# Kernel optimization log

Measured on AMD Instinct MI355X. Metric: run time of the kernel, lower is better.

## Reference

```python
import jax, jax.numpy as jnp
import numpy as np

N_NODES = 50000
N_EDGES = 600000
IN_F, HID, OUT_F = 602, 128, 41


def _gconv(x, W, b, src, dst, n):
    # DGL GraphConv, norm='both': D_dst^{-1/2} A (D_src^{-1/2} x W) + b
    ones = jnp.ones(src.shape, dtype=x.dtype)
    deg_out = jnp.clip(jax.ops.segment_sum(ones, src, num_segments=n), 1.0)
    deg_in = jnp.clip(jax.ops.segment_sum(ones, dst, num_segments=n), 1.0)
    h = x * jax.lax.rsqrt(deg_out)[:, None]
    h = h @ W  # dense transform first (in_feats > out_feats path)
    agg = jax.ops.segment_sum(h[src], dst, num_segments=n)  # [N, out]
    return agg * jax.lax.rsqrt(deg_in)[:, None] + b


def setup_inputs() -> dict:
    key = jax.random.key(0)
    ks = jax.random.split(key, 8)
    features = jax.random.normal(ks[0], (N_NODES, IN_F), dtype=jnp.float32)
    src = jax.random.randint(ks[1], (N_EDGES,), 0, N_NODES, dtype=jnp.int32)
    dst = jax.random.randint(ks[2], (N_EDGES,), 0, N_NODES, dtype=jnp.int32)
    def glorot(k, fan_in, fan_out):
        s = jnp.sqrt(6.0 / (fan_in + fan_out)).astype(jnp.float32)
        return jax.random.uniform(k, (fan_in, fan_out), jnp.float32, -s, s)
    return {
        'features': features, 'src': src, 'dst': dst,
        'W1': glorot(ks[3], IN_F, HID), 'b1': jnp.zeros((HID,), jnp.float32),
        'W2': glorot(ks[4], HID, HID), 'b2': jnp.zeros((HID,), jnp.float32),
        'W3': glorot(ks[5], HID, HID), 'b3': jnp.zeros((HID,), jnp.float32),
        'Wfc': glorot(ks[6], HID, OUT_F), 'bfc': jnp.zeros((OUT_F,), jnp.float32),
    }


def reference(features, src, dst, W1, b1, W2, b2, W3, b3, Wfc, bfc):
    n = features.shape[0]
    relu = jax.nn.relu
    x = relu(_gconv(features, W1, b1, src, dst, n))  # x = _x
    _x = relu(_gconv(x, W2, b2, src, dst, n))        # branch (layer2)
    x = relu(_gconv(x, W2, b2, src, dst, n))         # main (same layer2)
    x = relu(_gconv(x, W3, b3, src, dst, n))         # layer3
    x = relu(x + _x)                                  # residual + relu
    return x @ Wfc + bfc
```

## Files before the change

### kernel.cpp

```cpp
#include <hip/hip_runtime.h>
#include <hip/hip_bf16.h>

#define NN   50000
#define NE   600000
#define INF  602
#define HID  128
#define OUTF 41
#define NBLK 196

#define HISTB 2344
#define GEMMB 782

typedef __attribute__((ext_vector_type(8))) short bf16x8;
typedef __attribute__((ext_vector_type(4))) float f32x4;
typedef __attribute__((ext_vector_type(2))) float f32x2;

__device__ inline unsigned short f2bf(float x) {
    unsigned u = __float_as_uint(x);
    unsigned r = u + 0x7FFF + ((u >> 16) & 1);
    return (unsigned short)(r >> 16);
}

__device__ inline f32x2 up2(unsigned u) {
    return (f32x2){__uint_as_float(u << 16), __uint_as_float(u & 0xFFFF0000u)};
}

#define GLL16(gp, lp) \
    __builtin_amdgcn_global_load_lds((const __attribute__((address_space(1))) unsigned int*)(gp), \
                                     (__attribute__((address_space(3))) unsigned int*)(lp), 16, 0, 0)

__device__ inline void prep_w_body(const float* __restrict__ W, int K,
                                   unsigned short* __restrict__ out, int total4, int i) {
    if (i >= total4) return;
    int col = i & 127;
    int k4 = (i >> 7) << 2;
    short4 h;
    h.x = (short)f2bf((k4 + 0 < K) ? W[(size_t)(k4 + 0) * HID + col] : 0.f);
    h.y = (short)f2bf((k4 + 1 < K) ? W[(size_t)(k4 + 1) * HID + col] : 0.f);
    h.z = (short)f2bf((k4 + 2 < K) ? W[(size_t)(k4 + 2) * HID + col] : 0.f);
    h.w = (short)f2bf((k4 + 3 < K) ? W[(size_t)(k4 + 3) * HID + col] : 0.f);
    *(short4*)&out[(size_t)(k4 >> 3) * 1024 + col * 8 + (k4 & 7)] = h;
}

__global__ __launch_bounds__(256) void hist_prep_k(const int* __restrict__ src,
                                                   const int* __restrict__ dst,
                                                   int* __restrict__ cnt_out,
                                                   int* __restrict__ cnt_in,
                                                   const float* __restrict__ W1,
                                                   const float* __restrict__ W2,
                                                   const float* __restrict__ W3,
                                                   unsigned short* __restrict__ W1t,
                                                   unsigned short* __restrict__ W2t,
                                                   unsigned short* __restrict__ W3t) {
    int b = blockIdx.x;
    if (b < HISTB) {
        int e = b * 256 + threadIdx.x;
        if (e < NE) {
            atomicAdd(&cnt_out[src[e]], 1);
            atomicAdd(&cnt_in[dst[e]], 1);
        }
    } else {
        int b2 = b - HISTB;
        if (b2 < 80)       prep_w_body(W1, INF, W1t, 20480, b2 * 256 + threadIdx.x);
        else if (b2 < 96)  prep_w_body(W2, HID, W2t, 4096, (b2 - 80) * 256 + threadIdx.x);
        else               prep_w_body(W3, HID, W3t, 4096, (b2 - 96) * 256 + threadIdx.x);
    }
}

__global__ __launch_bounds__(256) void scan1_k(const int* __restrict__ cnt,
                                               int* __restrict__ rowptr,
                                               int* __restrict__ blockSum) {
    __shared__ int tmp[256];
    int tid = threadIdx.x;
    int i = blockIdx.x * 256 + tid;
    int v = (i < NN) ? cnt[i] : 0;
    tmp[tid] = v;
    __syncthreads();
#pragma unroll
    for (int off = 1; off < 256; off <<= 1) {
        int t = (tid >= off) ? tmp[tid - off] : 0;
        __syncthreads();
        tmp[tid] += t;
        __syncthreads();
    }
    if (i < NN) rowptr[i] = tmp[tid] - v;
    if (tid == 255) blockSum[blockIdx.x] = tmp[255];
}

__global__ __launch_bounds__(256) void scan23_k(int* __restrict__ rowptr,
                                                const int* __restrict__ blockSum,
                                                int* __restrict__ wcur,
                                                const int* __restrict__ cnt_out,
                                                const int* __restrict__ cnt_in,
                                                float* __restrict__ rs_out,
                                                float* __restrict__ rs_in) {
    const int tid = threadIdx.x;
    const int bid = blockIdx.x;
    int vAll = (tid < NBLK) ? blockSum[tid] : 0;
    int vPre = (tid < bid) ? vAll : 0;
#pragma unroll
    for (int o = 32; o; o >>= 1) {
        vAll += __shfl_down(vAll, o);
        vPre += __shfl_down(vPre, o);
    }
    __shared__ int sA[4], sP[4];
    if ((tid & 63) == 0) { sA[tid >> 6] = vAll; sP[tid >> 6] = vPre; }
    __syncthreads();
    int offAll = sA[0] + sA[1] + sA[2] + sA[3];
    int offPre = sP[0] + sP[1] + sP[2] + sP[3];
    int i = bid * 256 + tid;
    if (i < NN) {
        int r = rowptr[i] + offPre;
        rowptr[i] = r;
        wcur[i] = r;
        int co = cnt_out[i]; if (co < 1) co = 1;
        int ci = cnt_in[i];  if (ci < 1) ci = 1;
        rs_out[i] = rsqrtf((float)co);
        rs_in[i]  = rsqrtf((float)ci);
    }
    if (bid == NBLK - 1 && tid == 0) rowptr[NN] = offAll;
}

__global__ __launch_bounds__(256) void fill_gemm1_k(const int* __restrict__ src,
                                                    const int* __restrict__ dst,
                                                    int* __restrict__ wcur,
                                                    int* __restrict__ csrsrc,
                                                    const float* __restrict__ A,
                                                    const unsigned short* __restrict__ Wt,
                                                    const float* __restrict__ rs_out,
                                                    unsigned short* __restrict__ H, int n) {
    __shared__ __attribute__((aligned(16))) short As[64 * 136];
    __shared__ __attribute__((aligned(16))) short Bs[16 * 1024];

    if (blockIdx.x < HISTB) {
        int e = blockIdx.x * 256 + threadIdx.x;
        if (e < NE) {
            int p = atomicAdd(&wcur[dst[e]], 1);
            csrsrc[p] = src[e];
        }
        return;
    }

    const int gb = blockIdx.x - HISTB;
    const int tid = threadIdx.x;
    const int wave = tid >> 6;
    const int lane = tid & 63;
    const int quad = lane >> 4;
    const int l16 = lane & 15;
    const int rowBase = gb * 64;
    const int tileBase = rowBase + wave * 16;

    float4 apf[8];
    auto loadA = [&](int ch) {
        int kb = ch * 128;
#pragma unroll
        for (int c = 0; c < 8; ++c) {
            int f = c * 256 + tid;
            int row = f >> 5;
            int kc = (f & 31) << 2;
            int grow = rowBase + row;
            int gk = kb + kc;
            float4 v = {0.f, 0.f, 0.f, 0.f};
            if (grow < n) {
                if (gk + 3 < INF) {
                    v = *(const float4*)(A + (size_t)grow * INF + gk);
                } else {
                    if (gk + 0 < INF) v.x = A[(size_t)grow * INF + gk + 0];
                    if (gk + 1 < INF) v.y = A[(size_t)grow * INF + gk + 1];
                    if (gk + 2 < INF) v.z = A[(size_t)grow * INF + gk + 2];
                }
            }
            apf[c] = v;
        }
    };
    auto storeA = [&]() {
#pragma unroll
        for (int c = 0; c < 8; ++c) {
            int f = c * 256 + tid;
            int row = f >> 5;
            int kc = (f & 31) << 2;
            short4 h;
            h.x = (short)f2bf(apf[c].x); h.y = (short)f2bf(apf[c].y);
            h.z = (short)f2bf(apf[c].z); h.w = (short)f2bf(apf[c].w);
            *(short4*)&As[row * 136 + kc] = h;
        }
    };
    auto issueB = [&](int ch) {
#pragma unroll
        for (int c = 0; c < 8; ++c)
            GLL16(Wt + (size_t)ch * 16384 + c * 2048 + tid * 8, &Bs[c * 2048 + tid * 8]);
    };

    f32x4 acc[8];
#pragma unroll
    for (int j = 0; j < 8; ++j) acc[j] = (f32x4){0.f, 0.f, 0.f, 0.f};

    loadA(0);
    for (int ch = 0; ch < 5; ++ch) {
        __syncthreads();
        issueB(ch);
        storeA();
        __syncthreads();
        if (ch + 1 < 5) loadA(ch + 1);
#pragma unroll
        for (int s = 0; s < 4; ++s) {
            bf16x8 af = *(const bf16x8*)&As[(wave * 16 + l16) * 136 + s * 32 + quad * 8];
            const short* bg = &Bs[(s * 4 + quad) * 1024 + l16 * 8];
#pragma unroll
            for (int nt = 0; nt < 8; ++nt) {
                bf16x8 bf = *(const bf16x8*)(bg + nt * 128);
                acc[nt] = __builtin_amdgcn_mfma_f32_16x16x32_bf16(af, bf, acc[nt], 0, 0, 0);
            }
        }
    }

#pragma unroll
    for (int r = 0; r < 4; ++r) {
        int row = tileBase + quad * 4 + r;
        if (row < n) {
            float ro = rs_out[row];
#pragma unroll
            for (int nt = 0; nt < 8; ++nt)
                H[(size_t)row * HID + nt * 16 + l16] = f2bf(acc[nt][r] * ro);
        }
    }
}

__global__ __launch_bounds__(256) void gemm_hid_k(const unsigned short* __restrict__ A,
                                                  const unsigned short* __restrict__ Wt,
                                                  unsigned short* __restrict__ H, int n) {
    __shared__ __attribute__((aligned(16))) short As[64 * 136];
    __shared__ __attribute__((aligned(16))) short Bs[16384];

    const int tid = threadIdx.x;
    const int wave = tid >> 6;
    const int lane = tid & 63;
    const int quad = lane >> 4;
    const int l16 = lane & 15;
    const int wm = wave >> 1;
    const int wn = wave & 1;
    const int rowBase = blockIdx.x * 64;

#pragma unroll
    for (int c = 0; c < 8; ++c)
        GLL16(Wt + c * 2048 + tid * 8, &Bs[c * 2048 + tid * 8]);

#pragma unroll
    for (int c = 0; c < 4; ++c) {
        int f = c * 256 + tid;
        int row = f >> 4;
        int k16 = (f & 15) << 3;
        int grow = rowBase + row;
        int4 v = {0, 0, 0, 0};
        if (grow < n) v = *(const int4*)(A + (size_t)grow * HID + k16);
        *(int4*)&As[row * 136 + k16] = v;
    }
    __syncthreads();

    f32x4 acc[2][4];
#pragma unroll
    for (int i = 0; i < 2; ++i)
#pragma unroll
        for (int j = 0; j < 4; ++j) acc[i][j] = (f32x4){0.f, 0.f, 0.f, 0.f};

#pragma unroll
    for (int kq = 0; kq < 4; ++kq) {
        bf16x8 af[2], bfr[4];
#pragma unroll
        for (int mt = 0; mt < 2; ++mt)
            af[mt] = *(const bf16x8*)&As[(wm * 32 + mt * 16 + l16) * 136 + kq * 32 + quad * 8];
#pragma unroll
        for (int nt = 0; nt < 4; ++nt)
            bfr[nt] = *(const bf16x8*)&Bs[(kq * 4 + quad) * 1024 + (wn * 64 + nt * 16 + l16) * 8];
#pragma unroll
        for (int mt = 0; mt < 2; ++mt)
#pragma unroll
            for (int nt = 0; nt < 4; ++nt)
                acc[mt][nt] = __builtin_amdgcn_mfma_f32_16x16x32_bf16(af[mt], bfr[nt], acc[mt][nt], 0, 0, 0);
    }

#pragma unroll
    for (int mt = 0; mt < 2; ++mt)
#pragma unroll
        for (int r = 0; r < 4; ++r) {
            int row = rowBase + wm * 32 + mt * 16 + quad * 4 + r;
            if (row < n) {
#pragma unroll
                for (int nt = 0; nt < 4; ++nt) {
                    int col = wn * 64 + nt * 16 + l16;
                    H[(size_t)row * HID + col] = f2bf(acc[mt][nt][r]);
                }
            }
        }
}

__global__ __launch_bounds__(256) void gather_k(const unsigned short* __restrict__ H,
                                                const int* __restrict__ rowptr,
                                                const int* __restrict__ csrsrc,
                                                const float* __restrict__ rs_in,
                                                const float* __restrict__ rs_out,
                                                const float* __restrict__ bias,
                                                const float* __restrict__ resid,
                                                float* __restrict__ outX,
                                                unsigned short* __restrict__ outXs,
                                                int n) {
    const int lane = threadIdx.x & 63;
    const int g = lane >> 4;
    const int l = lane & 15;
    const int gbase = g << 4;
    const int wid = blockIdx.x * 4 + (threadIdx.x >> 6);
    const int node = wid * 4 + g;
    const bool alive = node < n;

    int beg = 0, end = 0;
    if (alive) { beg = rowptr[node]; end = rowptr[node + 1]; }

    f32x2 a01 = {0.f, 0.f}, a23 = {0.f, 0.f}, a45 = {0.f, 0.f}, a67 = {0.f, 0.f};

    for (int base = beg; base < end; base += 16) {
        int m = end - base; if (m > 16) m = 16;
        int idx = (l < m) ? csrsrc[base + l] : 0;
        int j = 0;
        for (; j + 3 < m; j += 4) {
            int s0 = __shfl(idx, gbase | j);
            int s1 = __shfl(idx, gbase | (j + 1));
            int s2 = __shfl(idx, gbase | (j + 2));
            int s3 = __shfl(idx, gbase | (j + 3));
            int4 u0 = *(const int4*)(H + (size_t)s0 * HID + l * 8);
            int4 u1 = *(const int4*)(H + (size_t)s1 * HID + l * 8);
            int4 u2 = *(const int4*)(H + (size_t)s2 * HID + l * 8);
            int4 u3 = *(const int4*)(H + (size_t)s3 * HID + l * 8);
#pragma unroll
            for (int q = 0; q < 4; ++q) {
                int4 u = (q == 0) ? u0 : (q == 1) ? u1 : (q == 2) ? u2 : u3;
                a01 += up2((unsigned)u.x);
                a23 += up2((unsigned)u.y);
                a45 += up2((unsigned)u.z);
                a67 += up2((unsigned)u.w);
            }
        }
        for (; j < m; ++j) {
            int s = __shfl(idx, gbase | j);
            int4 u = *(const int4*)(H + (size_t)s * HID + l * 8);
            a01 += up2((unsigned)u.x);
            a23 += up2((unsigned)u.y);
            a45 += up2((unsigned)u.z);
            a67 += up2((unsigned)u.w);
        }
    }

    if (!alive) return;

    float ri = rs_in[node];
    float4 b0 = *(const float4*)(bias + l * 8);
    float4 b1 = *(const float4*)(bias + l * 8 + 4);
    float v[8];
    v[0] = fmaxf(a01[0] * ri + b0.x, 0.f); v[1] = fmaxf(a01[1] * ri + b0.y, 0.f);
    v[2] = fmaxf(a23[0] * ri + b0.z, 0.f); v[3] = fmaxf(a23[1] * ri + b0.w, 0.f);
    v[4] = fmaxf(a45[0] * ri + b1.x, 0.f); v[5] = fmaxf(a45[1] * ri + b1.y, 0.f);
    v[6] = fmaxf(a67[0] * ri + b1.z, 0.f); v[7] = fmaxf(a67[1] * ri + b1.w, 0.f);

    size_t o = (size_t)node * HID + l * 8;
    if (resid) {
        float4 r0 = *(const float4*)(resid + o);
        float4 r1 = *(const float4*)(resid + o + 4);
        v[0] = fmaxf(v[0] + r0.x, 0.f); v[1] = fmaxf(v[1] + r0.y, 0.f);
        v[2] = fmaxf(v[2] + r0.z, 0.f); v[3] = fmaxf(v[3] + r0.w, 0.f);
        v[4] = fmaxf(v[4] + r1.x, 0.f); v[5] = fmaxf(v[5] + r1.y, 0.f);
        v[6] = fmaxf(v[6] + r1.z, 0.f); v[7] = fmaxf(v[7] + r1.w, 0.f);
    }
    if (outX) {
        *(float4*)(outX + o) = make_float4(v[0], v[1], v[2], v[3]);
        *(float4*)(outX + o + 4) = make_float4(v[4], v[5], v[6], v[7]);
    }
    if (outXs) {
        float ro = rs_out[node];
        int4 h;
        h.x = (int)(((unsigned)f2bf(v[1] * ro) << 16) | f2bf(v[0] * ro));
        h.y = (int)(((unsigned)f2bf(v[3] * ro) << 16) | f2bf(v[2] * ro));
        h.z = (int)(((unsigned)f2bf(v[5] * ro) << 16) | f2bf(v[4] * ro));
        h.w = (int)(((unsigned)f2bf(v[7] * ro) << 16) | f2bf(v[6] * ro));
        *(int4*)(outXs + o) = h;
    }
}

__global__ __launch_bounds__(256) void fc_k(const float* __restrict__ X,
                                            const float* __restrict__ Wfc,
                                            const float* __restrict__ bfc,
                                            float* __restrict__ out, int n) {
    __shared__ float Ws[HID * OUTF];
    __shared__ float Xs[4][HID];
    int tid = threadIdx.x;
    for (int i = tid; i < HID * OUTF; i += 256) Ws[i] = Wfc[i];
    int rowBase = blockIdx.x * 4;
    for (int i = tid; i < 4 * HID; i += 256) {
        int r = i >> 7, c = i & 127;
        int gr = rowBase + r;
        Xs[r][c] = (gr < n) ? X[(size_t)gr * HID + c] : 0.f;
    }
    __syncthreads();
    int wv = tid >> 6, lane = tid & 63;
    int row = rowBase + wv;
    if (row < n && lane < OUTF) {
        float acc = bfc[lane];
#pragma unroll 8
        for (int k = 0; k < HID; ++k) acc += Xs[wv][k] * Ws[k * OUTF + lane];
        out[(size_t)row * OUTF + lane] = acc;
    }
}

extern "C" void kernel_launch(void* const* d_in, const int* in_sizes, int n_in,
                              void* d_out, int out_size, void* d_ws, size_t ws_size,
                              hipStream_t stream) {
    const float* feat = (const float*)d_in[0];
    const int* src = (const int*)d_in[1];
    const int* dst = (const int*)d_in[2];
    const float* W1 = (const float*)d_in[3];
    const float* b1 = (const float*)d_in[4];
    const float* W2 = (const float*)d_in[5];
    const float* b2 = (const float*)d_in[6];
    const float* W3 = (const float*)d_in[7];
    const float* b3 = (const float*)d_in[8];
    const float* Wfc = (const float*)d_in[9];
    const float* bfc = (const float*)d_in[10];
    float* out = (float*)d_out;

    char* w = (char*)d_ws;
    auto alloc = [&](size_t b) -> void* {
        void* p = (void*)w;
        w += (b + 255) & ~(size_t)255;
        return p;
    };
    int* cnt = (int*)alloc(2 * NN * sizeof(int));
    int* cnt_out = cnt;
    int* cnt_in  = cnt + NN;
    int* rowptr  = (int*)alloc((NN + 1) * sizeof(int));
    int* wcur    = (int*)alloc(NN * sizeof(int));
    int* csrsrc  = (int*)alloc(NE * sizeof(int));
    int* blockSum = (int*)alloc(NBLK * sizeof(int));
    float* rs_out = (float*)alloc(NN * sizeof(float));
    float* rs_in  = (float*)alloc(NN * sizeof(float));
    unsigned short* W1t = (unsigned short*)alloc(10 * 8192 * sizeof(unsigned short));
    unsigned short* W2t = (unsigned short*)alloc(16384 * sizeof(unsigned short));
    unsigned short* W3t = (unsigned short*)alloc(16384 * sizeof(unsigned short));
    unsigned short* Ha = (unsigned short*)alloc((size_t)NN * HID * sizeof(unsigned short));
    unsigned short* Hb = (unsigned short*)alloc((size_t)NN * HID * sizeof(unsigned short));
    unsigned short* Xb = (unsigned short*)alloc((size_t)NN * HID * sizeof(unsigned short));
    float* resid = (float*)alloc((size_t)NN * HID * sizeof(float));
    float* Xfc   = (float*)alloc((size_t)NN * HID * sizeof(float));

    hipMemsetAsync(cnt, 0, 2 * NN * sizeof(int), stream);

    hist_prep_k<<<HISTB + 112, 256, 0, stream>>>(src, dst, cnt_out, cnt_in,
                                                 W1, W2, W3, W1t, W2t, W3t);
    scan1_k<<<NBLK, 256, 0, stream>>>(cnt_in, rowptr, blockSum);
    scan23_k<<<NBLK, 256, 0, stream>>>(rowptr, blockSum, wcur, cnt_out, cnt_in, rs_out, rs_in);
    fill_gemm1_k<<<HISTB + GEMMB, 256, 0, stream>>>(src, dst, wcur, csrsrc,
                                                    feat, W1t, rs_out, Ha, NN);

    const int ablk = (NN + 15) / 16;
    gather_k<<<ablk, 256, 0, stream>>>(Ha, rowptr, csrsrc, rs_in, rs_out, b1,
                                       nullptr, nullptr, Xb, NN);
    gemm_hid_k<<<GEMMB, 256, 0, stream>>>(Xb, W2t, Hb, NN);
    gather_k<<<ablk, 256, 0, stream>>>(Hb, rowptr, csrsrc, rs_in, rs_out, b2,
                                       nullptr, resid, Xb, NN);
    gemm_hid_k<<<GEMMB, 256, 0, stream>>>(Xb, W3t, Ha, NN);
    gather_k<<<ablk, 256, 0, stream>>>(Ha, rowptr, csrsrc, rs_in, rs_out, b3,
                                       resid, Xfc, nullptr, NN);
    fc_k<<<(NN + 3) / 4, 256, 0, stream>>>(Xfc, Wfc, bfc, out, NN);
}
```

Measured before the change: 442.2 us.

## Drop LDS staging in GEMM kernels; load MFMA fragments directly from global

Both the layer-1 GEMM (fused with the CSR fill) and the hidden-size GEMM now read A rows and pre-packed bf16 weights straight from global memory into MFMA operand registers. This removes the shared-memory tiles, the __syncthreads barriers and the async global-to-LDS weight copies. Each wave computes a full 16x128 output tile on its own. The cost is that every wave re-reads the whole weight matrix from L2/L1 instead of sharing it through LDS, and A rows are read with strided per-lane float4 loads that may coalesce poorly. The tail of K (602) is handled by a special last step.

```diff
diff --git a/kernel.cpp b/kernel.cpp
--- a/kernel.cpp
+++ b/kernel.cpp
@@ -21,13 +21,13 @@
     return (unsigned short)(r >> 16);
 }
 
+__device__ inline unsigned pack2bf(float lo, float hi) {
+    return ((unsigned)f2bf(hi) << 16) | f2bf(lo);
+}
+
 __device__ inline f32x2 up2(unsigned u) {
     return (f32x2){__uint_as_float(u << 16), __uint_as_float(u & 0xFFFF0000u)};
 }
-
-#define GLL16(gp, lp) \
-    __builtin_amdgcn_global_load_lds((const __attribute__((address_space(1))) unsigned int*)(gp), \
-                                     (__attribute__((address_space(3))) unsigned int*)(lp), 16, 0, 0)
 
 __device__ inline void prep_w_body(const float* __restrict__ W, int K,
                                    unsigned short* __restrict__ out, int total4, int i) {
@@ -129,9 +129,6 @@
                                                     const unsigned short* __restrict__ Wt,
                                                     const float* __restrict__ rs_out,
                                                     unsigned short* __restrict__ H, int n) {
-    __shared__ __attribute__((aligned(16))) short As[64 * 136];
-    __shared__ __attribute__((aligned(16))) short Bs[16 * 1024];
-
     if (blockIdx.x < HISTB) {
         int e = blockIdx.x * 256 + threadIdx.x;
         if (e < NE) {
@@ -147,70 +144,51 @@
     const int lane = tid & 63;
     const int quad = lane >> 4;
     const int l16 = lane & 15;
-    const int rowBase = gb * 64;
-    const int tileBase = rowBase + wave * 16;
-
-    float4 apf[8];
-    auto loadA = [&](int ch) {
-        int kb = ch * 128;
-#pragma unroll
-        for (int c = 0; c < 8; ++c) {
-            int f = c * 256 + tid;
-            int row = f >> 5;
-            int kc = (f & 31) << 2;
-            int grow = rowBase + row;
-            int gk = kb + kc;
-            float4 v = {0.f, 0.f, 0.f, 0.f};
-            if (grow < n) {
-                if (gk + 3 < INF) {
-                    v = *(const float4*)(A + (size_t)grow * INF + gk);
-                } else {
-                    if (gk + 0 < INF) v.x = A[(size_t)grow * INF + gk + 0];
-                    if (gk + 1 < INF) v.y = A[(size_t)grow * INF + gk + 1];
-                    if (gk + 2 < INF) v.z = A[(size_t)grow * INF + gk + 2];
-                }
-            }
-            apf[c] = v;
-        }
-    };
-    auto storeA = [&]() {
-#pragma unroll
-        for (int c = 0; c < 8; ++c) {
-            int f = c * 256 + tid;
-            int row = f >> 5;
-            int kc = (f & 31) << 2;
-            short4 h;
-            h.x = (short)f2bf(apf[c].x); h.y = (short)f2bf(apf[c].y);
-            h.z = (short)f2bf(apf[c].z); h.w = (short)f2bf(apf[c].w);
-            *(short4*)&As[row * 136 + kc] = h;
-        }
-    };
-    auto issueB = [&](int ch) {
-#pragma unroll
-        for (int c = 0; c < 8; ++c)
-            GLL16(Wt + (size_t)ch * 16384 + c * 2048 + tid * 8, &Bs[c * 2048 + tid * 8]);
-    };
+    const int tileBase = gb * 64 + wave * 16;
+
+    const int arow_i = tileBase + l16;
+    const float* __restrict__ arow = A + (size_t)(arow_i < n ? arow_i : 0) * INF;
 
     f32x4 acc[8];
 #pragma unroll
     for (int j = 0; j < 8; ++j) acc[j] = (f32x4){0.f, 0.f, 0.f, 0.f};
 
-    loadA(0);
-    for (int ch = 0; ch < 5; ++ch) {
-        __syncthreads();
-        issueB(ch);
-        storeA();
-        __syncthreads();
-        if (ch + 1 < 5) loadA(ch + 1);
-#pragma unroll
-        for (int s = 0; s < 4; ++s) {
-            bf16x8 af = *(const bf16x8*)&As[(wave * 16 + l16) * 136 + s * 32 + quad * 8];
-            const short* bg = &Bs[(s * 4 + quad) * 1024 + l16 * 8];
-#pragma unroll
-            for (int nt = 0; nt < 8; ++nt) {
-                bf16x8 bf = *(const bf16x8*)(bg + nt * 128);
-                acc[nt] = __builtin_amdgcn_mfma_f32_16x16x32_bf16(af, bf, acc[nt], 0, 0, 0);
-            }
+    for (int kg = 0; kg < 18; ++kg) {
+        int kb = kg * 32 + quad * 8;
+        float4 va = *(const float4*)(arow + kb);
+        float4 vb = *(const float4*)(arow + kb + 4);
+        union { bf16x8 v; unsigned u[4]; } af;
+        af.u[0] = pack2bf(va.x, va.y);
+        af.u[1] = pack2bf(va.z, va.w);
+        af.u[2] = pack2bf(vb.x, vb.y);
+        af.u[3] = pack2bf(vb.z, vb.w);
+        const unsigned short* bg = Wt + (size_t)(kg * 4 + quad) * 1024 + l16 * 8;
+#pragma unroll
+        for (int nt = 0; nt < 8; ++nt) {
+            bf16x8 bf = *(const bf16x8*)(bg + nt * 128);
+            acc[nt] = __builtin_amdgcn_mfma_f32_16x16x32_bf16(af.v, bf, acc[nt], 0, 0, 0);
+        }
+    }
+    {
+        int kb = 576 + quad * 8;
+        float4 va = {0.f, 0.f, 0.f, 0.f}, vb = {0.f, 0.f, 0.f, 0.f};
+        if (quad < 3) {
+            va = *(const float4*)(arow + kb);
+            vb = *(const float4*)(arow + kb + 4);
+        } else {
+            va.x = arow[600];
+            va.y = arow[601];
+        }
+        union { bf16x8 v; unsigned u[4]; } af;
+        af.u[0] = pack2bf(va.x, va.y);
+        af.u[1] = pack2bf(va.z, va.w);
+        af.u[2] = pack2bf(vb.x, vb.y);
+        af.u[3] = pack2bf(vb.z, vb.w);
+        const unsigned short* bg = Wt + (size_t)(18 * 4 + quad) * 1024 + l16 * 8;
+#pragma unroll
+        for (int nt = 0; nt < 8; ++nt) {
+            bf16x8 bf = *(const bf16x8*)(bg + nt * 128);
+            acc[nt] = __builtin_amdgcn_mfma_f32_16x16x32_bf16(af.v, bf, acc[nt], 0, 0, 0);
         }
     }
 
@@ -229,69 +207,40 @@
 __global__ __launch_bounds__(256) void gemm_hid_k(const unsigned short* __restrict__ A,
                                                   const unsigned short* __restrict__ Wt,
                                                   unsigned short* __restrict__ H, int n) {
-    __shared__ __attribute__((aligned(16))) short As[64 * 136];
-    __shared__ __attribute__((aligned(16))) short Bs[16384];
-
     const int tid = threadIdx.x;
     const int wave = tid >> 6;
     const int lane = tid & 63;
     const int quad = lane >> 4;
     const int l16 = lane & 15;
-    const int wm = wave >> 1;
-    const int wn = wave & 1;
-    const int rowBase = blockIdx.x * 64;
-
-#pragma unroll
-    for (int c = 0; c < 8; ++c)
-        GLL16(Wt + c * 2048 + tid * 8, &Bs[c * 2048 + tid * 8]);
-
-#pragma unroll
-    for (int c = 0; c < 4; ++c) {
-        int f = c * 256 + tid;
-        int row = f >> 4;
-        int k16 = (f & 15) << 3;
-        int grow = rowBase + row;
-        int4 v = {0, 0, 0, 0};
-        if (grow < n) v = *(const int4*)(A + (size_t)grow * HID + k16);
-        *(int4*)&As[row * 136 + k16] = v;
-    }
-    __syncthreads();
-
-    f32x4 acc[2][4];
-#pragma unroll
-    for (int i = 0; i < 2; ++i)
-#pragma unroll
-        for (int j = 0; j < 4; ++j) acc[i][j] = (f32x4){0.f, 0.f, 0.f, 0.f};
+    const int tileBase = blockIdx.x * 64 + wave * 16;
+
+    const int arow_i = tileBase + l16;
+    const unsigned short* __restrict__ arow = A + (size_t)(arow_i < n ? arow_i : 0) * HID;
+
+    f32x4 acc[8];
+#pragma unroll
+    for (int j = 0; j < 8; ++j) acc[j] = (f32x4){0.f, 0.f, 0.f, 0.f};
 
 #pragma unroll
     for (int kq = 0; kq < 4; ++kq) {
-        bf16x8 af[2], bfr[4];
-#pragma unroll
-        for (int mt = 0; mt < 2; ++mt)
-            af[mt] = *(const bf16x8*)&As[(wm * 32 + mt * 16 + l16) * 136 + kq * 32 + quad * 8];
-#pragma unroll
-        for (int nt = 0; nt < 4; ++nt)
-            bfr[nt] = *(const bf16x8*)&Bs[(kq * 4 + quad) * 1024 + (wn * 64 + nt * 16 + l16) * 8];
-#pragma unroll
-        for (int mt = 0; mt < 2; ++mt)
-#pragma unroll
-            for (int nt = 0; nt < 4; ++nt)
-                acc[mt][nt] = __builtin_amdgcn_mfma_f32_16x16x32_bf16(af[mt], bfr[nt], acc[mt][nt], 0, 0, 0);
-    }
-
-#pragma unroll
-    for (int mt = 0; mt < 2; ++mt)
-#pragma unroll
-        for (int r = 0; r < 4; ++r) {
-            int row = rowBase + wm * 32 + mt * 16 + quad * 4 + r;
-            if (row < n) {
-#pragma unroll
-                for (int nt = 0; nt < 4; ++nt) {
-                    int col = wn * 64 + nt * 16 + l16;
-                    H[(size_t)row * HID + col] = f2bf(acc[mt][nt][r]);
-                }
-            }
-        }
+        bf16x8 af = *(const bf16x8*)(arow + kq * 32 + quad * 8);
+        const unsigned short* bg = Wt + (size_t)(kq * 4 + quad) * 1024 + l16 * 8;
+#pragma unroll
+        for (int nt = 0; nt < 8; ++nt) {
+            bf16x8 bf = *(const bf16x8*)(bg + nt * 128);
+            acc[nt] = __builtin_amdgcn_mfma_f32_16x16x32_bf16(af, bf, acc[nt], 0, 0, 0);
+        }
+    }
+
+#pragma unroll
+    for (int r = 0; r < 4; ++r) {
+        int row = tileBase + quad * 4 + r;
+        if (row < n) {
+#pragma unroll
+            for (int nt = 0; nt < 8; ++nt)
+                H[(size_t)row * HID + nt * 16 + l16] = f2bf(acc[nt][r]);
+        }
+    }
 }
 
 __global__ __launch_bounds__(256) void gather_k(const unsigned short* __restrict__ H,
```

Measured after the change: 472.1 us. 1.07x slower.

## Stream first-layer GEMM operands from global into registers without LDS staging

Applied to the files above, without the earlier changes.

The first-layer feature GEMM no longer stages A and W tiles in shared memory behind block barriers. Each lane now loads its own fp32 A fragments straight from global memory, with a three-deep register prefetch across K-groups. It converts them to bf16 in registers and reads the bf16 W fragments directly from global/cache for each MFMA. This removes the LDS writes, the __syncthreads pairs and the LDS footprint, which should raise occupancy. The cost is that every wave now re-reads the whole weight matrix through the cache hierarchy, and the A loads are less coalesced.

```diff
diff --git a/kernel.cpp b/kernel.cpp
--- a/kernel.cpp
+++ b/kernel.cpp
@@ -19,6 +19,10 @@
     unsigned u = __float_as_uint(x);
     unsigned r = u + 0x7FFF + ((u >> 16) & 1);
     return (unsigned short)(r >> 16);
+}
+
+__device__ inline unsigned pack2bf(float lo, float hi) {
+    return ((unsigned)f2bf(hi) << 16) | f2bf(lo);
 }
 
 __device__ inline f32x2 up2(unsigned u) {
@@ -129,9 +133,6 @@
                                                     const unsigned short* __restrict__ Wt,
                                                     const float* __restrict__ rs_out,
                                                     unsigned short* __restrict__ H, int n) {
-    __shared__ __attribute__((aligned(16))) short As[64 * 136];
-    __shared__ __attribute__((aligned(16))) short Bs[16 * 1024];
-
     if (blockIdx.x < HISTB) {
         int e = blockIdx.x * 256 + threadIdx.x;
         if (e < NE) {
@@ -147,72 +148,60 @@
     const int lane = tid & 63;
     const int quad = lane >> 4;
     const int l16 = lane & 15;
-    const int rowBase = gb * 64;
-    const int tileBase = rowBase + wave * 16;
-
-    float4 apf[8];
-    auto loadA = [&](int ch) {
-        int kb = ch * 128;
-#pragma unroll
-        for (int c = 0; c < 8; ++c) {
-            int f = c * 256 + tid;
-            int row = f >> 5;
-            int kc = (f & 31) << 2;
-            int grow = rowBase + row;
-            int gk = kb + kc;
-            float4 v = {0.f, 0.f, 0.f, 0.f};
-            if (grow < n) {
-                if (gk + 3 < INF) {
-                    v = *(const float4*)(A + (size_t)grow * INF + gk);
-                } else {
-                    if (gk + 0 < INF) v.x = A[(size_t)grow * INF + gk + 0];
-                    if (gk + 1 < INF) v.y = A[(size_t)grow * INF + gk + 1];
-                    if (gk + 2 < INF) v.z = A[(size_t)grow * INF + gk + 2];
-                }
-            }
-            apf[c] = v;
+    const int tileBase = gb * 64 + wave * 16;
+
+    const int arow_i = tileBase + l16;
+    const float* __restrict__ arow = A + (size_t)(arow_i < n ? arow_i : 0) * INF;
+
+    f32x4 acc[8];
+#pragma unroll
+    for (int j = 0; j < 8; ++j) acc[j] = (f32x4){0.f, 0.f, 0.f, 0.f};
+
+    auto step = [&](float4& va, float4& vb, int kgUse, int kgRef, bool doRef) {
+        union { bf16x8 v; unsigned u[4]; } af;
+        af.u[0] = pack2bf(va.x, va.y);
+        af.u[1] = pack2bf(va.z, va.w);
+        af.u[2] = pack2bf(vb.x, vb.y);
+        af.u[3] = pack2bf(vb.z, vb.w);
+        if (doRef) {
+            const float* p = arow + kgRef * 32 + quad * 8;
+            va = *(const float4*)p;
+            vb = *(const float4*)(p + 4);
+        }
+        const unsigned short* bg = Wt + (size_t)(kgUse * 4 + quad) * 1024 + l16 * 8;
+#pragma unroll
+        for (int nt = 0; nt < 8; ++nt) {
+            bf16x8 bf = *(const bf16x8*)(bg + nt * 128);
+            acc[nt] = __builtin_amdgcn_mfma_f32_16x16x32_bf16(af.v, bf, acc[nt], 0, 0, 0);
         }
     };
-    auto storeA = [&]() {
-#pragma unroll
-        for (int c = 0; c < 8; ++c) {
-            int f = c * 256 + tid;
-            int row = f >> 5;
-            int kc = (f & 31) << 2;
-            short4 h;
-            h.x = (short)f2bf(apf[c].x); h.y = (short)f2bf(apf[c].y);
-            h.z = (short)f2bf(apf[c].z); h.w = (short)f2bf(apf[c].w);
-            *(short4*)&As[row * 136 + kc] = h;
-        }
-    };
-    auto issueB = [&](int ch) {
-#pragma unroll
-        for (int c = 0; c < 8; ++c)
-            GLL16(Wt + (size_t)ch * 16384 + c * 2048 + tid * 8, &Bs[c * 2048 + tid * 8]);
-    };
-
-    f32x4 acc[8];
-#pragma unroll
-    for (int j = 0; j < 8; ++j) acc[j] = (f32x4){0.f, 0.f, 0.f, 0.f};
-
-    loadA(0);
-    for (int ch = 0; ch < 5; ++ch) {
-        __syncthreads();
-        issueB(ch);
-        storeA();
-        __syncthreads();
-        if (ch + 1 < 5) loadA(ch + 1);
-#pragma unroll
-        for (int s = 0; s < 4; ++s) {
-            bf16x8 af = *(const bf16x8*)&As[(wave * 16 + l16) * 136 + s * 32 + quad * 8];
-            const short* bg = &Bs[(s * 4 + quad) * 1024 + l16 * 8];
-#pragma unroll
-            for (int nt = 0; nt < 8; ++nt) {
-                bf16x8 bf = *(const bf16x8*)(bg + nt * 128);
-                acc[nt] = __builtin_amdgcn_mfma_f32_16x16x32_bf16(af, bf, acc[nt], 0, 0, 0);
-            }
-        }
-    }
+
+    float4 a0, b0, a1, b1, a2, b2;
+    {
+        const float* p0 = arow + quad * 8;
+        a0 = *(const float4*)p0;            b0 = *(const float4*)(p0 + 4);
+        a1 = *(const float4*)(p0 + 32);     b1 = *(const float4*)(p0 + 36);
+        a2 = *(const float4*)(p0 + 64);     b2 = *(const float4*)(p0 + 68);
+    }
+    for (int i = 0; i < 5; ++i) {
+        step(a0, b0, 3 * i,     3 * i + 3, true);
+        step(a1, b1, 3 * i + 1, 3 * i + 4, true);
+        step(a2, b2, 3 * i + 2, 3 * i + 5, true);
+    }
+    step(a0, b0, 15, 0, false);
+    {
+        int kb = 576 + quad * 8;
+        if (quad < 3) {
+            a0 = *(const float4*)(arow + kb);
+            b0 = *(const float4*)(arow + kb + 4);
+        } else {
+            a0 = make_float4(arow[600], arow[601], 0.f, 0.f);
+            b0 = make_float4(0.f, 0.f, 0.f, 0.f);
+        }
+    }
+    step(a1, b1, 16, 0, false);
+    step(a2, b2, 17, 0, false);
+    step(a0, b0, 18, 0, false);
 
 #pragma unroll
     for (int r = 0; r < 4; ++r) {
```

Result: no change. 442.9 us (+0.2%).
